# Kernel tuning notes

Measured on AMD Instinct MI355X. Metric: run time of the kernel, lower is better.

The kernel has to match this reference:

```python
import jax, jax.numpy as jnp
import numpy as np

# Geometry of the single LocallyConnected2d layer being decomposed
FACTOR = 2      # number of sublayers the out_channels are split into
KH = KW = 3     # kernel size
DH = DW = 1     # stride
OH = OW = 32    # output spatial size
B, C_IN, C_OUT = 128, 32, 64
H = W = OH + KH - 1  # 34 (valid unfold with stride 1)


def setup_inputs() -> dict:
    key = jax.random.key(0)
    kx, kw_, kb = jax.random.split(key, 3)
    x = jax.random.normal(kx, (B, C_IN, H, W), dtype=jnp.float32)
    # per-location weights: (out_ch, in_ch, oh, ow, kh*kw) -- no weight sharing
    weight = jax.random.normal(kw_, (C_OUT, C_IN, OH, OW, KH * KW), dtype=jnp.float32) * 0.05
    bias = jax.random.normal(kb, (C_OUT, OH, OW), dtype=jnp.float32)
    return {"x": x, "weight": weight, "bias": bias}


def _unfold(x):
    # x: (B, C, H, W) -> patches: (B, C, OH, OW, KH*KW)
    # equivalent to torch x.unfold(2,kh,dh).unfold(3,kw,dw).reshape(..., kh*kw)
    cols = [x[:, :, i:i + DH * OH:DH, j:j + DW * OW:DW]
            for i in range(KH) for j in range(KW)]
    return jnp.stack(cols, axis=-1)


def reference(x, weight, bias):
    patches = _unfold(x)  # (B, C, OH, OW, K2)
    new_ch = weight.shape[0] // FACTOR
    outs = []
    for g in range(FACTOR):  # decomposed sublayers, concatenated on channel dim
        w_g = weight[g * new_ch:(g + 1) * new_ch]
        b_g = bias[g * new_ch:(g + 1) * new_ch]
        # out[b,o,i,j] = sum_{c,k} patches[b,c,i,j,k] * w[o,c,i,j,k] + b[o,i,j]
        o_g = jnp.einsum('bcijk,ocijk->boij', patches, w_g) + b_g[None]
        outs.append(o_g)
    return jnp.concatenate(outs, axis=1)  # (B, C_OUT, OH, OW)
```

## Files before the change

### kernel.cpp

```cpp
#include <hip/hip_runtime.h>
#include <cstdint>
#include <cstddef>

#define B_    128
#define C_    32
#define O_    64
#define H_    34
#define NPOS  1024
#define K9    9
#define BC    (B_ * C_)
#define BO    (B_ * O_)

typedef __bf16 v8bf __attribute__((ext_vector_type(8)));
typedef float  v4f  __attribute__((ext_vector_type(4)));
typedef float  f2u  __attribute__((ext_vector_type(2), aligned(4)));

__device__ __forceinline__ unsigned short f2bf(float f) {
    union { float f; unsigned int u; } v; v.f = f;
    unsigned int u = v.u;
    return (unsigned short)((u + 0x7FFFu + ((u >> 16) & 1u)) >> 16);
}
__device__ __forceinline__ float bf2f(unsigned short s) {
    union { unsigned int u; float f; } v; v.u = ((unsigned int)s) << 16;
    return v.f;
}

__global__ __launch_bounds__(256) void repack_x(const float* __restrict__ x,
                                                unsigned short* __restrict__ x2) {
    const int ph = blockIdx.x;
    const int b0 = (ph / H_) * 2;
    const int h  = ph % H_;
    __shared__ unsigned short tile[2][C_][H_ + 2];
    const int t = threadIdx.x;
    for (int e = t; e < 2 * C_ * H_; e += 256) {
        const int bb = e / (C_ * H_);
        const int rem = e % (C_ * H_);
        const int c = rem / H_, w = rem % H_;
        tile[bb][c][w] = f2bf(x[(((size_t)(b0 + bb) * C_ + c) * H_ + h) * H_ + w]);
    }
    __syncthreads();
    for (int e = t; e < H_ * 64; e += 256) {
        const int w = e >> 6;
        const int idx = e & 63;
        x2[((size_t)(h * H_ + w)) * BC + b0 * C_ + idx] = tile[idx >> 5][idx & 31][w];
    }
}

__global__ __launch_bounds__(256, 4) void lc_fused(const unsigned short* __restrict__ x2,
                                                   const float* __restrict__ weight,
                                                   const float* __restrict__ bias,
                                                   unsigned short* __restrict__ ws) {
    __shared__ __align__(16) unsigned short Wl[36 * 512];

    const int bid = blockIdx.x;
    const int jq = bid & 7;
    const int i  = (bid >> 3) & 31;
    const int oq = bid >> 8;
    const int j0 = jq * 4;
    const int o0 = oq * 16;
    const int posbase = i * 32 + j0;
    const int t = threadIdx.x;

    const float* wbase = weight + ((size_t)(o0 * C_) * NPOS + posbase) * K9;
#pragma unroll
    for (int r = 0; r < 36; ++r) {
        const int idx = r * 256 + t;
        const int pl = idx / 18;
        const int d2 = idx % 18;
        const f2u v = *(const f2u*)(wbase + (size_t)pl * (NPOS * K9) + d2 * 2);
        const int d = d2 * 2;
        Wl[d * 512 + pl]       = f2bf(v[0]);
        Wl[(d + 1) * 512 + pl] = f2bf(v[1]);
    }
    __syncthreads();

    const int wv = t >> 6;
    const int l  = t & 63;
    const int lm = l & 15;
    const int q  = l >> 4;

    v4f acc[4][2];
#pragma unroll
    for (int a = 0; a < 4; ++a)
#pragma unroll
        for (int m = 0; m < 2; ++m) acc[a][m] = (v4f){0.f, 0.f, 0.f, 0.f};

#pragma unroll
    for (int tap = 0; tap < K9; ++tap) {
        const int kh = tap / 3, kw = tap % 3;
        const int rowbase = (i + kh) * H_ + j0 + kw;
#pragma unroll
        for (int jj = 0; jj < 4; ++jj) {
            const v8bf bfr = *(const v8bf*)&Wl[(jj * K9 + tap) * 512 + lm * C_ + q * 8];
            const unsigned short* xrow = x2 + (size_t)(rowbase + jj) * BC;
            const v8bf af0 = *(const v8bf*)(xrow + (wv * 32 + lm) * C_ + q * 8);
            const v8bf af1 = *(const v8bf*)(xrow + (wv * 32 + 16 + lm) * C_ + q * 8);
            acc[jj][0] = __builtin_amdgcn_mfma_f32_16x16x32_bf16(af0, bfr, acc[jj][0], 0, 0, 0);
            acc[jj][1] = __builtin_amdgcn_mfma_f32_16x16x32_bf16(af1, bfr, acc[jj][1], 0, 0, 0);
        }
    }

#pragma unroll
    for (int jj = 0; jj < 4; ++jj) {
        const int pos = posbase + jj;
        const float bv = bias[(size_t)(o0 + lm) * NPOS + pos];
        unsigned short* wp = ws + (size_t)pos * BO + (o0 + lm) * B_;
#pragma unroll
        for (int mt = 0; mt < 2; ++mt) {
            const int b = wv * 32 + mt * 16 + q * 4;
            ushort4 pk;
            pk.x = f2bf(acc[jj][mt][0] + bv);
            pk.y = f2bf(acc[jj][mt][1] + bv);
            pk.z = f2bf(acc[jj][mt][2] + bv);
            pk.w = f2bf(acc[jj][mt][3] + bv);
            *(ushort4*)(wp + b) = pk;
        }
    }
}

__global__ __launch_bounds__(256) void lc_fallback(const float* __restrict__ x,
                                                   const float* __restrict__ weight,
                                                   const float* __restrict__ bias,
                                                   float* __restrict__ out) {
    const int pos = blockIdx.x;
    const int i = pos >> 5, j = pos & 31;
    const int t  = threadIdx.x;
    const int wv = t >> 6;
    const int l  = t & 63;
    const int lm = l & 15;
    const int q  = l >> 4;

    float bv[4];
#pragma unroll
    for (int nt = 0; nt < 4; ++nt)
        bv[nt] = bias[(size_t)(nt * 16 + lm) * NPOS + pos];

    v4f acc[2][4];
#pragma unroll
    for (int a = 0; a < 2; ++a)
#pragma unroll
        for (int n = 0; n < 4; ++n) acc[a][n] = (v4f){0.f, 0.f, 0.f, 0.f};

    for (int k = 0; k < K9; ++k) {
        const int kh = k / 3, kw = k % 3;
        v8bf af[2], bfr[4];
#pragma unroll
        for (int mt = 0; mt < 2; ++mt) {
            const int b = wv * 32 + mt * 16 + lm;
            union { v8bf v; unsigned short s[8]; } u;
#pragma unroll
            for (int cc = 0; cc < 8; ++cc)
                u.s[cc] = f2bf(x[(((size_t)b * C_ + q * 8 + cc) * H_ + (i + kh)) * H_ + (j + kw)]);
            af[mt] = u.v;
        }
#pragma unroll
        for (int nt = 0; nt < 4; ++nt) {
            union { v8bf v; unsigned short s[8]; } u;
#pragma unroll
            for (int cc = 0; cc < 8; ++cc) {
                const int p = (nt * 16 + lm) * C_ + q * 8 + cc;
                u.s[cc] = f2bf(weight[((size_t)p * NPOS + pos) * K9 + k]);
            }
            bfr[nt] = u.v;
        }
#pragma unroll
        for (int mt = 0; mt < 2; ++mt)
#pragma unroll
            for (int nt = 0; nt < 4; ++nt)
                acc[mt][nt] = __builtin_amdgcn_mfma_f32_16x16x32_bf16(
                    af[mt], bfr[nt], acc[mt][nt], 0, 0, 0);
    }
#pragma unroll
    for (int mt = 0; mt < 2; ++mt)
#pragma unroll
        for (int nt = 0; nt < 4; ++nt) {
            const int o = nt * 16 + lm;
#pragma unroll
            for (int r = 0; r < 4; ++r) {
                const int b = wv * 32 + mt * 16 + q * 4 + r;
                out[(size_t)(b * O_ + o) * NPOS + pos] = acc[mt][nt][r] + bv[nt];
            }
        }
}

__global__ __launch_bounds__(256) void transpose_out(const unsigned short* __restrict__ ws,
                                                     float* __restrict__ out) {
    __shared__ float tile[64][65];
    const int tb = blockIdx.x;
    const int o  = tb >> 5;
    const int bt = (tb >> 4) & 1;
    const int pt = tb & 15;
    const int b0 = bt * 64;
    const int p0 = pt * 64;
    const int tx = threadIdx.x & 63;
    const int ty = threadIdx.x >> 6;
#pragma unroll
    for (int r = 0; r < 16; ++r) {
        const int pr = r * 4 + ty;
        tile[pr][tx] = bf2f(ws[(size_t)(p0 + pr) * BO + o * B_ + b0 + tx]);
    }
    __syncthreads();
#pragma unroll
    for (int r = 0; r < 16; ++r) {
        const int br = r * 4 + ty;
        out[((size_t)(b0 + br) * O_ + o) * NPOS + p0 + tx] = tile[tx][br];
    }
}

extern "C" void kernel_launch(void* const* d_in, const int* in_sizes, int n_in,
                              void* d_out, int out_size, void* d_ws, size_t ws_size,
                              hipStream_t stream) {
    const float* x      = (const float*)d_in[0];
    const float* weight = (const float*)d_in[1];
    const float* bias   = (const float*)d_in[2];
    float* out          = (float*)d_out;

    const size_t WSB = (size_t)NPOS * BO * sizeof(unsigned short);
    const size_t X2B = (size_t)H_ * H_ * BC * sizeof(unsigned short);

    if (ws_size >= WSB + X2B) {
        unsigned short* wsout = (unsigned short*)d_ws;
        unsigned short* x2 = (unsigned short*)((char*)d_ws + WSB);
        repack_x<<<(B_ / 2) * H_, 256, 0, stream>>>(x, x2);
        lc_fused<<<1024, 256, 0, stream>>>(x2, weight, bias, wsout);
        transpose_out<<<2048, 256, 0, stream>>>(wsout, out);
    } else {
        lc_fallback<<<NPOS, 256, 0, stream>>>(x, weight, bias, out);
    }
}
```

Before: 167.8 us.

## Reuse x fragments across kw taps, swizzle weight LDS, vectorize weight loads

```diff
diff --git a/kernel.cpp b/kernel.cpp
--- a/kernel.cpp
+++ b/kernel.cpp
@@ -13,7 +13,7 @@
 
 typedef __bf16 v8bf __attribute__((ext_vector_type(8)));
 typedef float  v4f  __attribute__((ext_vector_type(4)));
-typedef float  f2u  __attribute__((ext_vector_type(2), aligned(4)));
+typedef float  f4a  __attribute__((ext_vector_type(4)));
 
 __device__ __forceinline__ unsigned short f2bf(float f) {
     union { float f; unsigned int u; } v; v.f = f;
@@ -48,7 +48,6 @@
 
 __global__ __launch_bounds__(256, 4) void lc_fused(const unsigned short* __restrict__ x2,
                                                    const float* __restrict__ weight,
-                                                   const float* __restrict__ bias,
                                                    unsigned short* __restrict__ ws) {
     __shared__ __align__(16) unsigned short Wl[36 * 512];
 
@@ -63,14 +62,15 @@
 
     const float* wbase = weight + ((size_t)(o0 * C_) * NPOS + posbase) * K9;
 #pragma unroll
-    for (int r = 0; r < 36; ++r) {
+    for (int r = 0; r < 18; ++r) {
         const int idx = r * 256 + t;
-        const int pl = idx / 18;
-        const int d2 = idx % 18;
-        const f2u v = *(const f2u*)(wbase + (size_t)pl * (NPOS * K9) + d2 * 2);
-        const int d = d2 * 2;
-        Wl[d * 512 + pl]       = f2bf(v[0]);
-        Wl[(d + 1) * 512 + pl] = f2bf(v[1]);
+        const int pl = idx / 9;
+        const int d4 = idx % 9;
+        const f4a v = *(const f4a*)(wbase + (size_t)pl * (NPOS * K9) + d4 * 4);
+        const int sw = ((pl >> 3) ^ (d4 & 7)) * 8 + (pl & 7);
+#pragma unroll
+        for (int u = 0; u < 4; ++u)
+            Wl[(d4 * 4 + u) * 512 + sw] = f2bf(v[u]);
     }
     __syncthreads();
 
@@ -86,33 +86,43 @@
         for (int m = 0; m < 2; ++m) acc[a][m] = (v4f){0.f, 0.f, 0.f, 0.f};
 
 #pragma unroll
-    for (int tap = 0; tap < K9; ++tap) {
-        const int kh = tap / 3, kw = tap % 3;
-        const int rowbase = (i + kh) * H_ + j0 + kw;
-#pragma unroll
-        for (int jj = 0; jj < 4; ++jj) {
-            const v8bf bfr = *(const v8bf*)&Wl[(jj * K9 + tap) * 512 + lm * C_ + q * 8];
-            const unsigned short* xrow = x2 + (size_t)(rowbase + jj) * BC;
-            const v8bf af0 = *(const v8bf*)(xrow + (wv * 32 + lm) * C_ + q * 8);
-            const v8bf af1 = *(const v8bf*)(xrow + (wv * 32 + 16 + lm) * C_ + q * 8);
-            acc[jj][0] = __builtin_amdgcn_mfma_f32_16x16x32_bf16(af0, bfr, acc[jj][0], 0, 0, 0);
-            acc[jj][1] = __builtin_amdgcn_mfma_f32_16x16x32_bf16(af1, bfr, acc[jj][1], 0, 0, 0);
+    for (int kh = 0; kh < 3; ++kh) {
+        v8bf ax[6][2];
+        const int rowbase = (i + kh) * H_ + j0;
+#pragma unroll
+        for (int w6 = 0; w6 < 6; ++w6) {
+            const unsigned short* xrow = x2 + (size_t)(rowbase + w6) * BC;
+            ax[w6][0] = *(const v8bf*)(xrow + (wv * 32 + lm) * C_ + q * 8);
+            ax[w6][1] = *(const v8bf*)(xrow + (wv * 32 + 16 + lm) * C_ + q * 8);
+        }
+#pragma unroll
+        for (int kw = 0; kw < 3; ++kw) {
+            const int tap = kh * 3 + kw;
+#pragma unroll
+            for (int jj = 0; jj < 4; ++jj) {
+                const int jk = jj * K9 + tap;
+                const int g  = ((lm * 4 + q) ^ ((jk >> 2) & 7)) * 8;
+                const v8bf bfr = *(const v8bf*)&Wl[jk * 512 + g];
+                acc[jj][0] = __builtin_amdgcn_mfma_f32_16x16x32_bf16(
+                    ax[kw + jj][0], bfr, acc[jj][0], 0, 0, 0);
+                acc[jj][1] = __builtin_amdgcn_mfma_f32_16x16x32_bf16(
+                    ax[kw + jj][1], bfr, acc[jj][1], 0, 0, 0);
+            }
         }
     }
 
 #pragma unroll
     for (int jj = 0; jj < 4; ++jj) {
         const int pos = posbase + jj;
-        const float bv = bias[(size_t)(o0 + lm) * NPOS + pos];
         unsigned short* wp = ws + (size_t)pos * BO + (o0 + lm) * B_;
 #pragma unroll
         for (int mt = 0; mt < 2; ++mt) {
             const int b = wv * 32 + mt * 16 + q * 4;
             ushort4 pk;
-            pk.x = f2bf(acc[jj][mt][0] + bv);
-            pk.y = f2bf(acc[jj][mt][1] + bv);
-            pk.z = f2bf(acc[jj][mt][2] + bv);
-            pk.w = f2bf(acc[jj][mt][3] + bv);
+            pk.x = f2bf(acc[jj][mt][0]);
+            pk.y = f2bf(acc[jj][mt][1]);
+            pk.z = f2bf(acc[jj][mt][2]);
+            pk.w = f2bf(acc[jj][mt][3]);
             *(ushort4*)(wp + b) = pk;
         }
     }
@@ -184,6 +194,7 @@
 }
 
 __global__ __launch_bounds__(256) void transpose_out(const unsigned short* __restrict__ ws,
+                                                     const float* __restrict__ bias,
                                                      float* __restrict__ out) {
     __shared__ float tile[64][65];
     const int tb = blockIdx.x;
@@ -199,11 +210,12 @@
         const int pr = r * 4 + ty;
         tile[pr][tx] = bf2f(ws[(size_t)(p0 + pr) * BO + o * B_ + b0 + tx]);
     }
+    const float bvt = bias[(size_t)o * NPOS + p0 + tx];
     __syncthreads();
 #pragma unroll
     for (int r = 0; r < 16; ++r) {
         const int br = r * 4 + ty;
-        out[((size_t)(b0 + br) * O_ + o) * NPOS + p0 + tx] = tile[tx][br];
+        out[((size_t)(b0 + br) * O_ + o) * NPOS + p0 + tx] = tile[tx][br] + bvt;
     }
 }
 
@@ -222,8 +234,8 @@
         unsigned short* wsout = (unsigned short*)d_ws;
         unsigned short* x2 = (unsigned short*)((char*)d_ws + WSB);
         repack_x<<<(B_ / 2) * H_, 256, 0, stream>>>(x, x2);
-        lc_fused<<<1024, 256, 0, stream>>>(x2, weight, bias, wsout);
-        transpose_out<<<2048, 256, 0, stream>>>(wsout, out);
+        lc_fused<<<1024, 256, 0, stream>>>(x2, weight, wsout);
+        transpose_out<<<2048, 256, 0, stream>>>(wsout, bias, out);
     } else {
         lc_fallback<<<NPOS, 256, 0, stream>>>(x, weight, bias, out);
     }
```

Result: no change. 164.7 us (-1.8%).
